# Kernel tuning notes

Hardware: AMD Instinct MI355X
Metric: run time of the kernel (lower is better)

## Reference

```python
import jax, jax.numpy as jnp
import numpy as np

QMAX = 127.0
QMIN = -128.0


def setup_inputs() -> dict:
    key = jax.random.key(0)
    k1, k2, k3 = jax.random.split(key, 3)
    B, N, D, O = 4, 4096, 2048, 2048
    x = jax.random.normal(k1, (B, N, D), dtype=jnp.float32)
    weight = jax.random.normal(k2, (O, D), dtype=jnp.float32)
    bias = jax.random.normal(k3, (O,), dtype=jnp.float32)
    return {"x": x, "weight": weight, "bias": bias}


def reference(x, weight, bias):
    # --- per-row symmetric int8 quantization of the weight [O, D] ---
    w_max = jnp.clip(jnp.max(jnp.abs(weight), axis=1, keepdims=True), 1e-8, None)
    w_scale = (w_max / QMAX)                     # [O, 1]
    w_q = jnp.clip(jnp.round(weight / w_scale), QMIN, QMAX).astype(jnp.int8)
    w_scale = w_scale.squeeze(1).astype(jnp.float32)  # [O]

    # --- dynamic per-row symmetric int8 quantization of x [B, N, D] ---
    x_max = jnp.max(jnp.abs(x), axis=2, keepdims=True)       # [B, N, 1]
    x_scale = jnp.maximum(x_max / QMAX, 1e-12)               # [B, N, 1]
    x_q = jnp.clip(jnp.round(x / x_scale), QMIN, QMAX).astype(jnp.int8)

    # --- int8 GEMM accumulated in int32: [B,N,D] x [O,D]^T -> [B,N,O] ---
    acc = jnp.einsum("bnd,od->bno", x_q.astype(jnp.int32), w_q.astype(jnp.int32))

    # --- dequantize with per-row activation scale and per-out-channel weight scale ---
    y = acc.astype(jnp.float32) * x_scale.astype(jnp.float32) * w_scale[None, None, :]
    y = y + bias
    return y.astype(x.dtype)
```

## Files before the change

kernel.cpp:

```cpp
#include <hip/hip_runtime.h>
#include <stdint.h>
#include <stddef.h>

typedef int v4i __attribute__((ext_vector_type(4)));

#define GLOAD_LDS16(g, l) __builtin_amdgcn_global_load_lds( \
    (const __attribute__((address_space(1))) void*)(g),     \
    (__attribute__((address_space(3))) void*)(l), 16, 0, 0)

__device__ __forceinline__ int pack4(float4 f, float s) {
    int a = (int)rintf(f.x / s); a = a < -128 ? -128 : (a > 127 ? 127 : a);
    int b = (int)rintf(f.y / s); b = b < -128 ? -128 : (b > 127 ? 127 : b);
    int c = (int)rintf(f.z / s); c = c < -128 ? -128 : (c > 127 ? 127 : c);
    int d = (int)rintf(f.w / s); d = d < -128 ? -128 : (d > 127 ? 127 : d);
    return (a & 255) | ((b & 255) << 8) | ((c & 255) << 16) | ((d & 255) << 24);
}

__global__ __launch_bounds__(256) void quant_rows_2048(
    const float* __restrict__ in, signed char* __restrict__ q,
    float* __restrict__ scales, float floorv)
{
    const int lane = threadIdx.x & 63;
    const int row  = blockIdx.x * 4 + (threadIdx.x >> 6);
    const float* rp = in + (size_t)row * 2048;

    float4 v[8];
#pragma unroll
    for (int j = 0; j < 2; ++j) {
        const float4* p = (const float4*)(rp + j * 1024 + lane * 16);
#pragma unroll
        for (int i = 0; i < 4; ++i) v[j * 4 + i] = p[i];
    }
    float am = 0.0f;
#pragma unroll
    for (int i = 0; i < 8; ++i) {
        am = fmaxf(am, fabsf(v[i].x));
        am = fmaxf(am, fabsf(v[i].y));
        am = fmaxf(am, fabsf(v[i].z));
        am = fmaxf(am, fabsf(v[i].w));
    }
#pragma unroll
    for (int off = 32; off; off >>= 1) am = fmaxf(am, __shfl_xor(am, off));
    const float s = fmaxf(am / 127.0f, floorv);

#pragma unroll
    for (int j = 0; j < 2; ++j) {
        int4 pk;
        pk.x = pack4(v[j * 4 + 0], s);
        pk.y = pack4(v[j * 4 + 1], s);
        pk.z = pack4(v[j * 4 + 2], s);
        pk.w = pack4(v[j * 4 + 3], s);
        *(int4*)(q + (size_t)row * 2048 + j * 1024 + lane * 16) = pk;
    }
    if (lane == 0) scales[row] = s;
}

__global__ __launch_bounds__(512, 2) void gemm_i8_pipe(
    const signed char* __restrict__ xq, const signed char* __restrict__ wq,
    const float* __restrict__ xs, const float* __restrict__ ws,
    const float* __restrict__ bias, float* __restrict__ out, int K)
{
    __shared__ __align__(16) signed char lds[131072];

    const int tid  = threadIdx.x;
    const int lane = tid & 63;
    const int wid  = tid >> 6;
    const int wm   = wid >> 2;
    const int wn   = wid & 3;

    const int nwg  = gridDim.x * gridDim.y;
    int orig = blockIdx.y * gridDim.x + blockIdx.x;
    int swz  = ((nwg & 7) == 0) ? ((orig & 7) * (nwg >> 3) + (orig >> 3)) : orig;
    const int brow = (swz / gridDim.x) * 256;
    const int bcol = (swz % gridDim.x) * 256;

    const int srow = tid >> 2;
    const int gch  = (((tid & 3) ^ ((tid >> 3) & 3)) << 4);
    const int lofs = tid << 4;
    const signed char* gA = xq + (size_t)(brow + srow) * K;
    const signed char* gB = wq + (size_t)(bcol + srow) * K;

#define ST_A(tt, half) GLOAD_LDS16(gA + (size_t)(half) * 128 * K + (size_t)(tt) * 64 + gch, \
                                   lds + ((((tt) & 3) << 14) + ((half) << 13) + lofs))
#define ST_B(tt, half) GLOAD_LDS16(gB + (size_t)(half) * 128 * K + (size_t)(tt) * 64 + gch, \
                                   lds + (65536 + (((tt) & 3) << 14) + ((half) << 13) + lofs))

    const int rl   = lane & 15;
    const int ko   = lane >> 4;
    const int slot = ((ko ^ ((rl >> 1) & 3)) << 4);

#define FRAG_A(buf, r) (*(const v4i*)(lds + (((buf) << 14) + (r) * 64 + slot)))
#define FRAG_B(buf, r) (*(const v4i*)(lds + (65536 + ((buf) << 14) + (r) * 64 + slot)))

    v4i acc[8][4] = {};
    const int ar = wm * 128 + rl;
    const int br = wn * 64 + rl;

#define MFMA16(M0)                                                                      \
    do {                                                                                \
        __builtin_amdgcn_s_setprio(1);                                                  \
        _Pragma("unroll")                                                               \
        for (int mm = 0; mm < 4; ++mm) {                                                \
            acc[M0 + mm][0] = __builtin_amdgcn_mfma_i32_16x16x64_i8(af[mm], bc0, acc[M0 + mm][0], 0, 0, 0); \
            acc[M0 + mm][1] = __builtin_amdgcn_mfma_i32_16x16x64_i8(af[mm], bc1, acc[M0 + mm][1], 0, 0, 0); \
            acc[M0 + mm][2] = __builtin_amdgcn_mfma_i32_16x16x64_i8(af[mm], bc2, acc[M0 + mm][2], 0, 0, 0); \
            acc[M0 + mm][3] = __builtin_amdgcn_mfma_i32_16x16x64_i8(af[mm], bc3, acc[M0 + mm][3], 0, 0, 0); \
        }                                                                               \
        __builtin_amdgcn_s_setprio(0);                                                  \
    } while (0)

#define BAR()   __builtin_amdgcn_s_barrier()
#define LGKM0() do { asm volatile("s_waitcnt lgkmcnt(0)" ::: "memory"); \
                     __builtin_amdgcn_sched_barrier(0); } while (0)

    ST_A(0, 0); ST_A(0, 1); ST_B(0, 0); ST_B(0, 1);
    ST_A(1, 0); ST_A(1, 1); ST_B(1, 0); ST_B(1, 1);
    ST_A(2, 0); ST_A(2, 1); ST_B(2, 0); ST_B(2, 1);
    asm volatile("s_waitcnt vmcnt(8)" ::: "memory");
    BAR();

    const int NT = K >> 6;
    for (int t = 0; t < NT; ++t) {
        const int buf = t & 3;
        const bool st = (t + 3 < NT);
        v4i af[4];
        v4i bc0 = FRAG_B(buf, br);
        v4i bc1 = FRAG_B(buf, br + 16);
        v4i bc2 = FRAG_B(buf, br + 32);
        v4i bc3 = FRAG_B(buf, br + 48);
        af[0] = FRAG_A(buf, ar);
        af[1] = FRAG_A(buf, ar + 16);
        af[2] = FRAG_A(buf, ar + 32);
        af[3] = FRAG_A(buf, ar + 48);
        if (st) { ST_A(t + 3, 0); ST_A(t + 3, 1); }
        BAR(); LGKM0();
        MFMA16(0);
        BAR();
        af[0] = FRAG_A(buf, ar + 64);
        af[1] = FRAG_A(buf, ar + 80);
        af[2] = FRAG_A(buf, ar + 96);
        af[3] = FRAG_A(buf, ar + 112);
        if (st) { ST_B(t + 3, 0); ST_B(t + 3, 1); }
        BAR(); LGKM0();
        MFMA16(4);
        if (t <= NT - 4)      asm volatile("s_waitcnt vmcnt(8)" ::: "memory");
        else if (t == NT - 3) asm volatile("s_waitcnt vmcnt(4)" ::: "memory");
        else if (t == NT - 2) asm volatile("s_waitcnt vmcnt(0)" ::: "memory");
        BAR();
    }

    const int rg = lane >> 4;
#pragma unroll
    for (int n = 0; n < 4; ++n) {
        const int col = bcol + wn * 64 + n * 16 + rl;
        const float wsc = ws[col];
        const float bv  = bias[col];
#pragma unroll
        for (int m = 0; m < 8; ++m) {
#pragma unroll
            for (int j = 0; j < 4; ++j) {
                const int row = brow + wm * 128 + m * 16 + rg * 4 + j;
                out[(size_t)row * 2048 + col] =
                    (float)acc[m][n][j] * xs[row] * wsc + bv;
            }
        }
    }
#undef ST_A
#undef ST_B
#undef FRAG_A
#undef FRAG_B
#undef MFMA16
#undef BAR
#undef LGKM0
}

extern "C" void kernel_launch(void* const* d_in, const int* in_sizes, int n_in,
                              void* d_out, int out_size, void* d_ws, size_t ws_size,
                              hipStream_t stream) {
    const float* x    = (const float*)d_in[0];
    const float* w    = (const float*)d_in[1];
    const float* bias = (const float*)d_in[2];
    float* out = (float*)d_out;

    const int D = 2048;
    const int O = in_sizes[2];
    const int M = in_sizes[0] / D;

    char* wsb = (char*)d_ws;
    signed char* xq  = (signed char*)wsb;
    signed char* wqp = (signed char*)(wsb + (size_t)M * D);
    float* xs  = (float*)(wsb + (size_t)M * D + (size_t)O * D);
    float* wsc = (float*)(wsb + (size_t)M * D + (size_t)O * D + (size_t)M * 4);

    quant_rows_2048<<<M / 4, 256, 0, stream>>>(x, xq, xs, 1e-12f);
    quant_rows_2048<<<O / 4, 256, 0, stream>>>(w, wqp, wsc, 1e-8f / 127.0f);

    dim3 grid(O / 256, M / 256);
    gemm_i8_pipe<<<grid, 512, 0, stream>>>(xq, wqp, xs, wsc, bias, out, D);
}
```

Baseline: 129.2 us.

## Prefetch next tile's LDS fragments into registers during MFMA phases

Restructures the int8 GEMM main loop so register fragments for the next K-tile (B and first-half A) are read from LDS while the current tile's second-half MFMAs run, using partial lgkmcnt waits instead of full drains. The vmcnt waits are tightened so the next buffer is resident one iteration earlier. The aim is to hide LDS read latency behind matrix-core work, at the cost of extra live vector registers (which may cause spilling under the 2-waves launch bound) and volatile LDS reads, which could hinder compiler scheduling.

```diff
diff --git a/kernel.cpp b/kernel.cpp
--- a/kernel.cpp
+++ b/kernel.cpp
@@ -89,64 +89,83 @@
     const int ko   = lane >> 4;
     const int slot = ((ko ^ ((rl >> 1) & 3)) << 4);
 
-#define FRAG_A(buf, r) (*(const v4i*)(lds + (((buf) << 14) + (r) * 64 + slot)))
-#define FRAG_B(buf, r) (*(const v4i*)(lds + (65536 + ((buf) << 14) + (r) * 64 + slot)))
+#define FRAG_A(buf, r) (*(const volatile v4i*)(lds + (((buf) << 14) + (r) * 64 + slot)))
+#define FRAG_B(buf, r) (*(const volatile v4i*)(lds + (65536 + ((buf) << 14) + (r) * 64 + slot)))
 
     v4i acc[8][4] = {};
     const int ar = wm * 128 + rl;
     const int br = wn * 64 + rl;
 
-#define MFMA16(M0)                                                                      \
+#define MFMA16(MB, A0, A1, A2, A3)                                                      \
     do {                                                                                \
         __builtin_amdgcn_s_setprio(1);                                                  \
-        _Pragma("unroll")                                                               \
-        for (int mm = 0; mm < 4; ++mm) {                                                \
-            acc[M0 + mm][0] = __builtin_amdgcn_mfma_i32_16x16x64_i8(af[mm], bc0, acc[M0 + mm][0], 0, 0, 0); \
-            acc[M0 + mm][1] = __builtin_amdgcn_mfma_i32_16x16x64_i8(af[mm], bc1, acc[M0 + mm][1], 0, 0, 0); \
-            acc[M0 + mm][2] = __builtin_amdgcn_mfma_i32_16x16x64_i8(af[mm], bc2, acc[M0 + mm][2], 0, 0, 0); \
-            acc[M0 + mm][3] = __builtin_amdgcn_mfma_i32_16x16x64_i8(af[mm], bc3, acc[M0 + mm][3], 0, 0, 0); \
-        }                                                                               \
+        acc[MB+0][0] = __builtin_amdgcn_mfma_i32_16x16x64_i8(A0, bc0, acc[MB+0][0], 0, 0, 0); \
+        acc[MB+0][1] = __builtin_amdgcn_mfma_i32_16x16x64_i8(A0, bc1, acc[MB+0][1], 0, 0, 0); \
+        acc[MB+0][2] = __builtin_amdgcn_mfma_i32_16x16x64_i8(A0, bc2, acc[MB+0][2], 0, 0, 0); \
+        acc[MB+0][3] = __builtin_amdgcn_mfma_i32_16x16x64_i8(A0, bc3, acc[MB+0][3], 0, 0, 0); \
+        acc[MB+1][0] = __builtin_amdgcn_mfma_i32_16x16x64_i8(A1, bc0, acc[MB+1][0], 0, 0, 0); \
+        acc[MB+1][1] = __builtin_amdgcn_mfma_i32_16x16x64_i8(A1, bc1, acc[MB+1][1], 0, 0, 0); \
+        acc[MB+1][2] = __builtin_amdgcn_mfma_i32_16x16x64_i8(A1, bc2, acc[MB+1][2], 0, 0, 0); \
+        acc[MB+1][3] = __builtin_amdgcn_mfma_i32_16x16x64_i8(A1, bc3, acc[MB+1][3], 0, 0, 0); \
+        acc[MB+2][0] = __builtin_amdgcn_mfma_i32_16x16x64_i8(A2, bc0, acc[MB+2][0], 0, 0, 0); \
+        acc[MB+2][1] = __builtin_amdgcn_mfma_i32_16x16x64_i8(A2, bc1, acc[MB+2][1], 0, 0, 0); \
+        acc[MB+2][2] = __builtin_amdgcn_mfma_i32_16x16x64_i8(A2, bc2, acc[MB+2][2], 0, 0, 0); \
+        acc[MB+2][3] = __builtin_amdgcn_mfma_i32_16x16x64_i8(A2, bc3, acc[MB+2][3], 0, 0, 0); \
+        acc[MB+3][0] = __builtin_amdgcn_mfma_i32_16x16x64_i8(A3, bc0, acc[MB+3][0], 0, 0, 0); \
+        acc[MB+3][1] = __builtin_amdgcn_mfma_i32_16x16x64_i8(A3, bc1, acc[MB+3][1], 0, 0, 0); \
+        acc[MB+3][2] = __builtin_amdgcn_mfma_i32_16x16x64_i8(A3, bc2, acc[MB+3][2], 0, 0, 0); \
+        acc[MB+3][3] = __builtin_amdgcn_mfma_i32_16x16x64_i8(A3, bc3, acc[MB+3][3], 0, 0, 0); \
         __builtin_amdgcn_s_setprio(0);                                                  \
     } while (0)
 
-#define BAR()   __builtin_amdgcn_s_barrier()
-#define LGKM0() do { asm volatile("s_waitcnt lgkmcnt(0)" ::: "memory"); \
-                     __builtin_amdgcn_sched_barrier(0); } while (0)
+#define BAR()    __builtin_amdgcn_s_barrier()
+#define LGKM(N)  do { asm volatile("s_waitcnt lgkmcnt(" #N ")" ::: "memory"); \
+                      __builtin_amdgcn_sched_barrier(0); } while (0)
 
     ST_A(0, 0); ST_A(0, 1); ST_B(0, 0); ST_B(0, 1);
     ST_A(1, 0); ST_A(1, 1); ST_B(1, 0); ST_B(1, 1);
     ST_A(2, 0); ST_A(2, 1); ST_B(2, 0); ST_B(2, 1);
-    asm volatile("s_waitcnt vmcnt(8)" ::: "memory");
+    asm volatile("s_waitcnt vmcnt(4)" ::: "memory");
     BAR();
+
+    v4i bc0 = FRAG_B(0, br);
+    v4i bc1 = FRAG_B(0, br + 16);
+    v4i bc2 = FRAG_B(0, br + 32);
+    v4i bc3 = FRAG_B(0, br + 48);
+    v4i af0 = FRAG_A(0, ar);
+    v4i af1 = FRAG_A(0, ar + 16);
+    v4i af2 = FRAG_A(0, ar + 32);
+    v4i af3 = FRAG_A(0, ar + 48);
+    v4i an0, an1, an2, an3, bn0, bn1, bn2, bn3;
 
     const int NT = K >> 6;
     for (int t = 0; t < NT; ++t) {
-        const int buf = t & 3;
-        const bool st = (t + 3 < NT);
-        v4i af[4];
-        v4i bc0 = FRAG_B(buf, br);
-        v4i bc1 = FRAG_B(buf, br + 16);
-        v4i bc2 = FRAG_B(buf, br + 32);
-        v4i bc3 = FRAG_B(buf, br + 48);
-        af[0] = FRAG_A(buf, ar);
-        af[1] = FRAG_A(buf, ar + 16);
-        af[2] = FRAG_A(buf, ar + 32);
-        af[3] = FRAG_A(buf, ar + 48);
+        const int buf  = t & 3;
+        const int nbuf = (t + 1) & 3;
+        const bool st  = (t + 3 < NT);
+        an0 = FRAG_A(buf, ar + 64);
+        an1 = FRAG_A(buf, ar + 80);
+        an2 = FRAG_A(buf, ar + 96);
+        an3 = FRAG_A(buf, ar + 112);
         if (st) { ST_A(t + 3, 0); ST_A(t + 3, 1); }
-        BAR(); LGKM0();
-        MFMA16(0);
+        BAR(); LGKM(4);
+        MFMA16(0, af0, af1, af2, af3);
         BAR();
-        af[0] = FRAG_A(buf, ar + 64);
-        af[1] = FRAG_A(buf, ar + 80);
-        af[2] = FRAG_A(buf, ar + 96);
-        af[3] = FRAG_A(buf, ar + 112);
+        bn0 = FRAG_B(nbuf, br);
+        bn1 = FRAG_B(nbuf, br + 16);
+        bn2 = FRAG_B(nbuf, br + 32);
+        bn3 = FRAG_B(nbuf, br + 48);
+        af0 = FRAG_A(nbuf, ar);
+        af1 = FRAG_A(nbuf, ar + 16);
+        af2 = FRAG_A(nbuf, ar + 32);
+        af3 = FRAG_A(nbuf, ar + 48);
         if (st) { ST_B(t + 3, 0); ST_B(t + 3, 1); }
-        BAR(); LGKM0();
-        MFMA16(4);
-        if (t <= NT - 4)      asm volatile("s_waitcnt vmcnt(8)" ::: "memory");
-        else if (t == NT - 3) asm volatile("s_waitcnt vmcnt(4)" ::: "memory");
-        else if (t == NT - 2) asm volatile("s_waitcnt vmcnt(0)" ::: "memory");
+        BAR(); LGKM(8);
+        MFMA16(4, an0, an1, an2, an3);
+        if (t <= NT - 4)      asm volatile("s_waitcnt vmcnt(4)" ::: "memory");
+        else if (t == NT - 3) asm volatile("s_waitcnt vmcnt(0)" ::: "memory");
         BAR();
+        bc0 = bn0; bc1 = bn1; bc2 = bn2; bc3 = bn3;
     }
 
     const int rg = lane >> 4;
@@ -171,7 +190,7 @@
 #undef FRAG_B
 #undef MFMA16
 #undef BAR
-#undef LGKM0
+#undef LGKM
 }
 
 extern "C" void kernel_launch(void* const* d_in, const int* in_sizes, int n_in,
```

New measurement: 160.7 us. 24.4% more time.
